# Kernel tuning notes

Measured on AMD Instinct MI355X. Metric: run time of the kernel, lower is better.

Reference implementation:

```python
import jax, jax.numpy as jnp
import numpy as np

B, S, D = 8, 2048, 512
MINF = 20000.0  # matches tf code's -20000.0 mask constant


def setup_inputs() -> dict:
    key = jax.random.key(0)
    k1, k2, k3 = jax.random.split(key, 3)
    x1 = jax.random.normal(k1, (B, S, D), dtype=jnp.float32)
    x2 = jax.random.normal(k2, (B, S, D), dtype=jnp.float32)
    # glorot_normal init for the learned (S, S) positional kernel
    std = np.sqrt(2.0 / (S + S)).astype(np.float32)
    kernel = jax.random.normal(k3, (S, S), dtype=jnp.float32) * std
    return {"x1": x1, "x2": x2, "kernel": kernel}


def reference(x1, x2, kernel):
    S_ = kernel.shape[0]
    # tf.matmul(kernel, inputs[i]) broadcasts (S,S) @ (B,S,D) -> (B,S,D)
    h1 = jnp.einsum('st,btd->bsd', kernel, x1)
    h2 = jnp.einsum('st,btd->bsd', kernel, x2)
    # att_scores: (B, S, S)
    scores = jnp.einsum('bsd,btd->bst', h1, h2)
    d_k = jnp.asarray(S_, dtype=scores.dtype) ** 0.5
    # upper_m[i,j] = -20000 for j > i (strictly upper), else 0; added BEFORE scaling
    row = jnp.arange(S_)
    mask = jnp.where(row[None, :] > row[:, None], -MINF, 0.0).astype(scores.dtype)
    attn = jax.nn.softmax((scores + mask) / d_k, axis=-1)
    # note: output attends over h1 (not h2), as in the original code
    return jnp.einsum('bst,btd->bsd', attn, h1)
```

## Files before the change

kernel.cpp:

```cpp
#include <hip/hip_runtime.h>
#include <hip/hip_bf16.h>

#define S_DIM 2048
#define D_DIM 512
#define B_DIM 8
#define SCALE 0.02209708691207961f

typedef __hip_bfloat16 bf16;
typedef short bf16x8 __attribute__((ext_vector_type(8)));
typedef float f32x4 __attribute__((ext_vector_type(4)));

__device__ __forceinline__ unsigned short f2b(float f) {
  __hip_bfloat16 h = __float2bfloat16(f);
  return __builtin_bit_cast(unsigned short, h);
}
__device__ __forceinline__ float b2f(unsigned short s) {
  return __bfloat162float(__builtin_bit_cast(__hip_bfloat16, s));
}

__device__ __forceinline__ void load_lds16(const void* g, void* l) {
  __builtin_amdgcn_global_load_lds((const __attribute__((address_space(1))) void*)g,
                                   (__attribute__((address_space(3))) void*)l, 16, 0, 0);
}

__global__ void prep(const float* __restrict__ x1, const float* __restrict__ x2,
                     const float* __restrict__ km,
                     bf16* __restrict__ xt, bf16* __restrict__ Kbf,
                     float* __restrict__ rowsum) {
  const int z = blockIdx.z;
  const int tid = threadIdx.x;
  if (z == 16) {
    const int bid = blockIdx.y * 8 + blockIdx.x;
    const float4* p = (const float4*)km;
    bf16x8* o = (bf16x8*)Kbf;
#pragma unroll
    for (int it = 0; it < 8; it++) {
      int i = bid * 2048 + it * 256 + tid;
      float4 a = p[2 * i], b = p[2 * i + 1];
      bf16x8 r;
      r[0] = f2b(a.x); r[1] = f2b(a.y); r[2] = f2b(a.z); r[3] = f2b(a.w);
      r[4] = f2b(b.x); r[5] = f2b(b.y); r[6] = f2b(b.z); r[7] = f2b(b.w);
      o[i] = r;
    }
    if (bid < 8) {
      float4 zf = {0.0f, 0.0f, 0.0f, 0.0f};
      float4* rp = (float4*)(rowsum + bid * 2048);
      rp[tid * 2] = zf;
      rp[tid * 2 + 1] = zf;
    }
    return;
  }
  __shared__ unsigned short t[64][66];
  const float* in = (z < 8 ? x1 : x2) + (size_t)(z & 7) * (S_DIM * D_DIM);
  bf16* ob = xt + (size_t)z * (size_t)(D_DIM * S_DIM);
  const int r0 = blockIdx.y * 64;
  const int c0 = blockIdx.x * 64;
  const int lr = tid >> 4, lq = tid & 15;
#pragma unroll
  for (int i = 0; i < 4; i++) {
    int r = i * 16 + lr;
    float4 v = *(const float4*)(in + (size_t)(r0 + r) * D_DIM + c0 + lq * 4);
    t[lq * 4 + 0][r] = f2b(v.x);
    t[lq * 4 + 1][r] = f2b(v.y);
    t[lq * 4 + 2][r] = f2b(v.z);
    t[lq * 4 + 3][r] = f2b(v.w);
  }
  __syncthreads();
#pragma unroll
  for (int j = 0; j < 4; j++) {
    int d = j * 16 + lr;
    const unsigned short* p = &t[d][lq * 4];
    uint2 u;
    u.x = (unsigned)p[0] | ((unsigned)p[1] << 16);
    u.y = (unsigned)p[2] | ((unsigned)p[3] << 16);
    *(uint2*)(ob + (size_t)(c0 + d) * S_DIM + r0 + lq * 4) = u;
  }
}

__global__ __launch_bounds__(512, 1) void gemm_h(
    const bf16* __restrict__ A, const bf16* __restrict__ X, bf16* __restrict__ H) {
  extern __shared__ char smem[];
  const int pid = blockIdx.x;
  const int mt = pid & 7;
  const int r_ = pid >> 3;
  const int ntile = r_ & 1;
  const int item = r_ >> 1;
  const int m0 = mt * 256, n0 = ntile * 256;
  const bf16* Xi = X + (size_t)item * (D_DIM * S_DIM);
  bf16* Hi = H + (size_t)item * (S_DIM * D_DIM);

  const int tid = threadIdx.x;
  const int w = tid >> 6, L = tid & 63;
  const int l15 = L & 15, lhi = L >> 4;
  const int wr = w >> 2, wn = w & 3;

  const int srow = tid >> 3;
  const int sslot = ((tid & 7) ^ (srow & 7)) * 8;
  const bf16* pA[4];
  const bf16* pB[4];
#pragma unroll
  for (int ld = 0; ld < 4; ld++) {
    pA[ld] = A + (size_t)(m0 + ld * 64 + srow) * 2048 + sslot;
    pB[ld] = Xi + (size_t)(n0 + ld * 64 + srow) * 2048 + sslot;
  }

  auto stage = [&](int t) {
    char* dA = smem + (t & 1) * 32768 + w * 1024;
    char* dB = smem + 65536 + (t & 1) * 32768 + w * 1024;
    const int ko = t * 64;
#pragma unroll
    for (int ld = 0; ld < 4; ld++) {
      load_lds16(pA[ld] + ko, dA + ld * 8192);
      load_lds16(pB[ld] + ko, dB + ld * 8192);
    }
  };

  const int xsw = l15 & 7;
  int offA0[8], offB0[4];
#pragma unroll
  for (int m = 0; m < 8; m++)
    offA0[m] = (wr * 128 + m * 16 + l15) * 128 + ((lhi ^ xsw) << 4);
#pragma unroll
  for (int n = 0; n < 4; n++)
    offB0[n] = (wn * 64 + n * 16 + l15) * 128 + ((lhi ^ xsw) << 4);

  f32x4 acc[8][4];
#pragma unroll
  for (int m = 0; m < 8; m++)
#pragma unroll
    for (int n = 0; n < 4; n++) acc[m][n] = (f32x4){0, 0, 0, 0};

  stage(0);
  asm volatile("s_waitcnt vmcnt(0)" ::: "memory");
  __builtin_amdgcn_s_barrier();
  asm volatile("" ::: "memory");

#pragma unroll 1
  for (int t = 0; t < 32; ++t) {
    if (t + 1 < 32) stage(t + 1);
    const char* bA = smem + (t & 1) * 32768;
    const char* bB = smem + 65536 + (t & 1) * 32768;
#pragma unroll
    for (int kk = 0; kk < 2; kk++) {
      bf16x8 af[8], bfv[4];
#pragma unroll
      for (int m = 0; m < 8; m++) af[m] = *(const bf16x8*)(bA + (offA0[m] ^ (kk << 6)));
#pragma unroll
      for (int n = 0; n < 4; n++) bfv[n] = *(const bf16x8*)(bB + (offB0[n] ^ (kk << 6)));
      __builtin_amdgcn_s_setprio(1);
#pragma unroll
      for (int m = 0; m < 8; m++)
#pragma unroll
        for (int n = 0; n < 4; n++)
          acc[m][n] = __builtin_amdgcn_mfma_f32_16x16x32_bf16(bfv[n], af[m], acc[m][n], 0, 0, 0);
      __builtin_amdgcn_s_setprio(0);
    }
    asm volatile("s_waitcnt vmcnt(0)" ::: "memory");
    __builtin_amdgcn_s_barrier();
    asm volatile("" ::: "memory");
  }

#pragma unroll
  for (int m = 0; m < 8; m++) {
    int grow = m0 + wr * 128 + m * 16 + l15;
#pragma unroll
    for (int n = 0; n < 4; n++) {
      int gcol = n0 + wn * 64 + n * 16 + lhi * 4;
      uint2 u;
      u.x = ((unsigned)f2b(acc[m][n][1]) << 16) | f2b(acc[m][n][0]);
      u.y = ((unsigned)f2b(acc[m][n][3]) << 16) | f2b(acc[m][n][2]);
      *(uint2*)(Hi + (size_t)grow * D_DIM + gcol) = u;
    }
  }
}

__global__ __launch_bounds__(512, 2) void gemm_score(
    const bf16* __restrict__ H1, const bf16* __restrict__ H2,
    bf16* __restrict__ E, float* __restrict__ rowsum, bf16* __restrict__ H1T) {
  extern __shared__ char smem[];
  const int pid = blockIdx.x;
  const int tid = threadIdx.x;

  if (pid >= 288) {
    const int tb = pid - 288;
    const int half = tid >> 8;
    const int t5 = tid & 255;
    unsigned short (*tl)[66] = (unsigned short (*)[66])(smem + half * 8448);
    const int lr = t5 >> 4, lq = t5 & 15;
#pragma unroll 1
    for (int i = 0; i < 4; i++) {
      const int tile = tb * 8 + half * 4 + i;
      const int z = tile >> 8;
      const int rem = tile & 255;
      const int r0 = (rem >> 3) * 64;
      const int c0 = (rem & 7) * 64;
      const bf16* ib = H1 + (size_t)z * (S_DIM * D_DIM);
      bf16* ob = H1T + (size_t)z * (S_DIM * D_DIM);
#pragma unroll
      for (int j = 0; j < 4; j++) {
        int r = j * 16 + lr;
        uint2 v = *(const uint2*)(ib + (size_t)(r0 + r) * D_DIM + c0 + lq * 4);
        tl[lq * 4 + 0][r] = (unsigned short)(v.x & 0xffff);
        tl[lq * 4 + 1][r] = (unsigned short)(v.x >> 16);
        tl[lq * 4 + 2][r] = (unsigned short)(v.y & 0xffff);
        tl[lq * 4 + 3][r] = (unsigned short)(v.y >> 16);
      }
      __syncthreads();
#pragma unroll
      for (int j = 0; j < 4; j++) {
        int d = j * 16 + lr;
        const unsigned short* p = &tl[d][lq * 4];
        uint2 u;
        u.x = (unsigned)p[0] | ((unsigned)p[1] << 16);
        u.y = (unsigned)p[2] | ((unsigned)p[3] << 16);
        *(uint2*)(ob + (size_t)(c0 + d) * S_DIM + r0 + lq * 4) = u;
      }
      __syncthreads();
    }
    return;
  }

  const int b = pid & 7;
  const int tri = pid >> 3;
  int mt = (int)((sqrtf(8.0f * (float)tri + 1.0f) - 1.0f) * 0.5f);
  while ((mt + 1) * (mt + 2) / 2 <= tri) mt++;
  while (mt * (mt + 1) / 2 > tri) mt--;
  const int nt = tri - mt * (mt + 1) / 2;
  const int m0 = mt * 256, n0 = nt * 256;
  const bool diag = (mt == nt);
  const bf16* Ab = H1 + (size_t)b * S_DIM * D_DIM;
  const bf16* Bb = H2 + (size_t)b * S_DIM * D_DIM;
  bf16* Eb = E + (size_t)b * S_DIM * S_DIM;
  float* rs = rowsum + b * S_DIM;

  const int w = tid >> 6, L = tid & 63;
  const int l15 = L & 15, lhi = L >> 4;
  const int wr = w >> 2, wn = w & 3;

  const int srow = tid >> 2;
  const int sslot = ((tid & 3) ^ ((tid >> 3) & 3)) * 8;
  const bf16* pA[2];
  const bf16* pB[2];
#pragma unroll
  for (int ld = 0; ld < 2; ld++) {
    pA[ld] = Ab + (size_t)(m0 + ld * 128 + srow) * D_DIM + sslot;
    pB[ld] = Bb + (size_t)(n0 + ld * 128 + srow) * D_DIM + sslot;
  }

  auto stage = [&](int t) {
    char* dA = smem + (t & 1) * 16384;
    char* dB = smem + 32768 + (t & 1) * 16384;
#pragma unroll
    for (int ld = 0; ld < 2; ld++)
      load_lds16(pA[ld] + t * 32, dA + ld * 8192 + w * 1024);
#pragma unroll
    for (int ld = 0; ld < 2; ld++)
      load_lds16(pB[ld] + t * 32, dB + ld * 8192 + w * 1024);
  };

  const int xo = (lhi ^ ((l15 >> 1) & 3)) << 4;
  int offA[8], offB[4];
#pragma unroll
  for (int m = 0; m < 8; m++) offA[m] = (wr * 128 + m * 16 + l15) * 64 + xo;
#pragma unroll
  for (int n = 0; n < 4; n++) offB[n] = (wn * 64 + n * 16 + l15) * 64 + xo;

  f32x4 acc[8][4];
#pragma unroll
  for (int m = 0; m < 8; m++)
#pragma unroll
    for (int n = 0; n < 4; n++) acc[m][n] = (f32x4){0, 0, 0, 0};

  stage(0);
#pragma unroll 2
  for (int t = 0; t < 16; ++t) {
    __syncthreads();
    if (t + 1 < 16) stage(t + 1);
    const char* bA = smem + (t & 1) * 16384;
    const char* bB = smem + 32768 + (t & 1) * 16384;
    bf16x8 af[8], bfv[4];
#pragma unroll
    for (int m = 0; m < 8; m++) af[m] = *(const bf16x8*)(bA + offA[m]);
#pragma unroll
    for (int n = 0; n < 4; n++) bfv[n] = *(const bf16x8*)(bB + offB[n]);
    __builtin_amdgcn_s_setprio(1);
#pragma unroll
    for (int m = 0; m < 8; m++)
#pragma unroll
      for (int n = 0; n < 4; n++)
        acc[m][n] = __builtin_amdgcn_mfma_f32_16x16x32_bf16(bfv[n], af[m], acc[m][n], 0, 0, 0);
    __builtin_amdgcn_s_setprio(0);
  }

#pragma unroll
  for (int m = 0; m < 8; m++) {
    int sg = m0 + wr * 128 + m * 16 + l15;
    float rp = 0.0f;
#pragma unroll
    for (int n = 0; n < 4; n++) {
      int tg0 = n0 + wn * 64 + n * 16 + lhi * 4;
      unsigned short e[4];
#pragma unroll
      for (int r = 0; r < 4; r++) {
        float v = (!diag || (tg0 + r) <= sg) ? __expf(acc[m][n][r] * SCALE) : 0.0f;
        e[r] = f2b(v);
        rp += b2f(e[r]);
      }
      uint2 u;
      u.x = ((unsigned)e[1] << 16) | e[0];
      u.y = ((unsigned)e[3] << 16) | e[2];
      *(uint2*)(Eb + (size_t)sg * S_DIM + tg0) = u;
    }
    rp += __shfl_xor(rp, 16);
    rp += __shfl_xor(rp, 32);
    if (lhi == 0) atomicAdd(rs + sg, rp);
  }
}

__global__ __launch_bounds__(256, 2) void gemm_pv(
    const bf16* __restrict__ E, const bf16* __restrict__ H1T,
    const float* __restrict__ rowsum, float* __restrict__ out) {
  extern __shared__ char smem[];
  const int pid = blockIdx.x;
  const int b = pid & 7;
  const int r_ = pid >> 3;
  const int nt = r_ & 3;
  const int mb = r_ >> 2;
  const int mt = (mb < 8) ? 2 * mb : 31 - 2 * mb;
  const int m0 = mt * 128, n0 = nt * 128;
  const int NT = (mt + 1) * 4;
  const bf16* Ab = E + (size_t)b * S_DIM * S_DIM + (size_t)m0 * S_DIM;
  const bf16* Bb = H1T + (size_t)b * D_DIM * S_DIM + (size_t)n0 * S_DIM;
  const float* rs = rowsum + b * S_DIM;
  float* Cb = out + (size_t)b * S_DIM * D_DIM;

  const int tid = threadIdx.x;
  const int w = tid >> 6, L = tid & 63;
  const int l15 = L & 15, lhi = L >> 4;
  const int wr = w >> 1, wc = w & 1;

  const int srow = tid >> 2;
  const int sslot = ((tid & 3) ^ ((tid >> 3) & 3)) * 8;
  const bf16* pA[2];
  const bf16* pB[2];
#pragma unroll
  for (int ld = 0; ld < 2; ld++) {
    pA[ld] = Ab + (size_t)(ld * 64 + srow) * S_DIM + sslot;
    pB[ld] = Bb + (size_t)(ld * 64 + srow) * S_DIM + sslot;
  }

  char* A0 = smem;          char* A1 = smem + 8192;   char* A2 = smem + 16384;
  char* B0 = smem + 24576;  char* B1 = smem + 32768;  char* B2 = smem + 40960;

  auto stage = [&](int t2, char* dA, char* dB) {
#pragma unroll
    for (int ld = 0; ld < 2; ld++)
      load_lds16(pA[ld] + t2 * 32, dA + ld * 4096 + w * 1024);
#pragma unroll
    for (int ld = 0; ld < 2; ld++)
      load_lds16(pB[ld] + t2 * 32, dB + ld * 4096 + w * 1024);
  };

  const int xo = (lhi ^ ((l15 >> 1) & 3)) << 4;
  int offA[4], offB[4];
#pragma unroll
  for (int m = 0; m < 4; m++) offA[m] = (wr * 64 + m * 16 + l15) * 64 + xo;
#pragma unroll
  for (int n = 0; n < 4; n++) offB[n] = (wc * 64 + n * 16 + l15) * 64 + xo;

  f32x4 acc[4][4];
#pragma unroll
  for (int m = 0; m < 4; m++)
#pragma unroll
    for (int n = 0; n < 4; n++) acc[m][n] = (f32x4){0, 0, 0, 0};

  stage(0, A0, B0);
  stage(1, A1, B1);

#pragma unroll 1
  for (int t = 0; t < NT; ++t) {
    if (t < NT - 1) asm volatile("s_waitcnt vmcnt(4)" ::: "memory");
    else            asm volatile("s_waitcnt vmcnt(0)" ::: "memory");
    __builtin_amdgcn_s_barrier();
    asm volatile("" ::: "memory");
    if (t + 2 < NT) stage(t + 2, A2, B2);

    bf16x8 af[4], bfv[4];
#pragma unroll
    for (int m = 0; m < 4; m++) af[m] = *(const bf16x8*)(A0 + offA[m]);
#pragma unroll
    for (int n = 0; n < 4; n++) bfv[n] = *(const bf16x8*)(B0 + offB[n]);
    __builtin_amdgcn_s_setprio(1);
#pragma unroll
    for (int m = 0; m < 4; m++)
#pragma unroll
      for (int n = 0; n < 4; n++)
        acc[m][n] = __builtin_amdgcn_mfma_f32_16x16x32_bf16(bfv[n], af[m], acc[m][n], 0, 0, 0);
    __builtin_amdgcn_s_setprio(0);

    char* tA = A0; A0 = A1; A1 = A2; A2 = tA;
    char* tB = B0; B0 = B1; B1 = B2; B2 = tB;
  }

#pragma unroll
  for (int m = 0; m < 4; m++) {
    int sg = m0 + wr * 64 + m * 16 + l15;
    float inv = 1.0f / rs[sg];
#pragma unroll
    for (int n = 0; n < 4; n++) {
      int gcol = n0 + wc * 64 + n * 16 + lhi * 4;
      float4 o;
      o.x = acc[m][n][0] * inv;
      o.y = acc[m][n][1] * inv;
      o.z = acc[m][n][2] * inv;
      o.w = acc[m][n][3] * inv;
      *(float4*)(Cb + (size_t)sg * D_DIM + gcol) = o;
    }
  }
}

extern "C" void kernel_launch(void* const* d_in, const int* in_sizes, int n_in,
                              void* d_out, int out_size, void* d_ws, size_t ws_size,
                              hipStream_t stream) {
  const float* x1 = (const float*)d_in[0];
  const float* x2 = (const float*)d_in[1];
  const float* km = (const float*)d_in[2];
  float* out = (float*)d_out;
  char* ws = (char*)d_ws;
  bf16* E    = (bf16*)(ws);
  bf16* Kbf  = (bf16*)(ws);
  bf16* x1t  = (bf16*)(ws + (8ull << 20));
  bf16* h1n  = (bf16*)(ws + (64ull << 20));
  bf16* h2n  = (bf16*)(ws + (80ull << 20));
  bf16* h1t  = (bf16*)(ws + (96ull << 20));
  float* rowsum = (float*)(ws + (112ull << 20));

  prep<<<dim3(8, 32, 17), 256, 0, stream>>>(x1, x2, km, x1t, Kbf, rowsum);
  gemm_h<<<256, 512, 131072, stream>>>(Kbf, x1t, h1n);
  gemm_score<<<544, 512, 65536, stream>>>(h1n, h2n, E, rowsum, h1t);
  gemm_pv<<<512, 256, 49152, stream>>>(E, h1t, rowsum, out);
}
```

Measured before the change: 163.3 us.

## Use BK=64 double-buffered pipeline in gemm_pv with wider LDS swizzle

The P·V GEMM now stages K-tiles of 64 instead of 32, halving the number of loop iterations and barriers. The triple-buffered BK=32 prefetch is replaced by double buffering, with loads issued before compute and a full vmcnt(0) wait plus barrier at the end of each iteration. The LDS swizzle widens to an 8-slot XOR pattern for 128-byte rows. Shared memory grows from 48 KB to 64 KB per block, and prefetch depth drops to one tile, which may expose more load latency.

```diff
diff --git a/kernel.cpp b/kernel.cpp
--- a/kernel.cpp
+++ b/kernel.cpp
@@ -328,7 +328,7 @@
   const int mb = r_ >> 2;
   const int mt = (mb < 8) ? 2 * mb : 31 - 2 * mb;
   const int m0 = mt * 128, n0 = nt * 128;
-  const int NT = (mt + 1) * 4;
+  const int NT = (mt + 1) * 2;
   const bf16* Ab = E + (size_t)b * S_DIM * S_DIM + (size_t)m0 * S_DIM;
   const bf16* Bb = H1T + (size_t)b * D_DIM * S_DIM + (size_t)n0 * S_DIM;
   const float* rs = rowsum + b * S_DIM;
@@ -339,34 +339,35 @@
   const int l15 = L & 15, lhi = L >> 4;
   const int wr = w >> 1, wc = w & 1;
 
-  const int srow = tid >> 2;
-  const int sslot = ((tid & 3) ^ ((tid >> 3) & 3)) * 8;
-  const bf16* pA[2];
-  const bf16* pB[2];
-#pragma unroll
-  for (int ld = 0; ld < 2; ld++) {
-    pA[ld] = Ab + (size_t)(ld * 64 + srow) * S_DIM + sslot;
-    pB[ld] = Bb + (size_t)(ld * 64 + srow) * S_DIM + sslot;
-  }
-
-  char* A0 = smem;          char* A1 = smem + 8192;   char* A2 = smem + 16384;
-  char* B0 = smem + 24576;  char* B1 = smem + 32768;  char* B2 = smem + 40960;
-
-  auto stage = [&](int t2, char* dA, char* dB) {
-#pragma unroll
-    for (int ld = 0; ld < 2; ld++)
-      load_lds16(pA[ld] + t2 * 32, dA + ld * 4096 + w * 1024);
-#pragma unroll
-    for (int ld = 0; ld < 2; ld++)
-      load_lds16(pB[ld] + t2 * 32, dB + ld * 4096 + w * 1024);
+  const int srow = tid >> 3;
+  const int sslot = ((tid & 7) ^ (srow & 7)) * 8;
+  const bf16* pA[4];
+  const bf16* pB[4];
+#pragma unroll
+  for (int ld = 0; ld < 4; ld++) {
+    pA[ld] = Ab + (size_t)(ld * 32 + srow) * S_DIM + sslot;
+    pB[ld] = Bb + (size_t)(ld * 32 + srow) * S_DIM + sslot;
+  }
+
+  auto stage = [&](int t) {
+    char* dA = smem + (t & 1) * 16384 + w * 1024;
+    char* dB = smem + 32768 + (t & 1) * 16384 + w * 1024;
+    const int ko = t * 64;
+#pragma unroll
+    for (int ld = 0; ld < 4; ld++) {
+      load_lds16(pA[ld] + ko, dA + ld * 4096);
+      load_lds16(pB[ld] + ko, dB + ld * 4096);
+    }
   };
 
-  const int xo = (lhi ^ ((l15 >> 1) & 3)) << 4;
-  int offA[4], offB[4];
-#pragma unroll
-  for (int m = 0; m < 4; m++) offA[m] = (wr * 64 + m * 16 + l15) * 64 + xo;
-#pragma unroll
-  for (int n = 0; n < 4; n++) offB[n] = (wc * 64 + n * 16 + l15) * 64 + xo;
+  const int xsw = l15 & 7;
+  int offA0[4], offB0[4];
+#pragma unroll
+  for (int m = 0; m < 4; m++)
+    offA0[m] = (wr * 64 + m * 16 + l15) * 128 + ((lhi ^ xsw) << 4);
+#pragma unroll
+  for (int n = 0; n < 4; n++)
+    offB0[n] = (wc * 64 + n * 16 + l15) * 128 + ((lhi ^ xsw) << 4);
 
   f32x4 acc[4][4];
 #pragma unroll
@@ -374,32 +375,34 @@
 #pragma unroll
     for (int n = 0; n < 4; n++) acc[m][n] = (f32x4){0, 0, 0, 0};
 
-  stage(0, A0, B0);
-  stage(1, A1, B1);
+  stage(0);
+  asm volatile("s_waitcnt vmcnt(0)" ::: "memory");
+  __builtin_amdgcn_s_barrier();
+  asm volatile("" ::: "memory");
 
 #pragma unroll 1
   for (int t = 0; t < NT; ++t) {
-    if (t < NT - 1) asm volatile("s_waitcnt vmcnt(4)" ::: "memory");
-    else            asm volatile("s_waitcnt vmcnt(0)" ::: "memory");
+    if (t + 1 < NT) stage(t + 1);
+    const char* bA = smem + (t & 1) * 16384;
+    const char* bB = smem + 32768 + (t & 1) * 16384;
+#pragma unroll
+    for (int kk = 0; kk < 2; kk++) {
+      bf16x8 af[4], bfv[4];
+#pragma unroll
+      for (int m = 0; m < 4; m++) af[m] = *(const bf16x8*)(bA + (offA0[m] ^ (kk << 6)));
+#pragma unroll
+      for (int n = 0; n < 4; n++) bfv[n] = *(const bf16x8*)(bB + (offB0[n] ^ (kk << 6)));
+      __builtin_amdgcn_s_setprio(1);
+#pragma unroll
+      for (int m = 0; m < 4; m++)
+#pragma unroll
+        for (int n = 0; n < 4; n++)
+          acc[m][n] = __builtin_amdgcn_mfma_f32_16x16x32_bf16(bfv[n], af[m], acc[m][n], 0, 0, 0);
+      __builtin_amdgcn_s_setprio(0);
+    }
+    asm volatile("s_waitcnt vmcnt(0)" ::: "memory");
     __builtin_amdgcn_s_barrier();
     asm volatile("" ::: "memory");
-    if (t + 2 < NT) stage(t + 2, A2, B2);
-
-    bf16x8 af[4], bfv[4];
-#pragma unroll
-    for (int m = 0; m < 4; m++) af[m] = *(const bf16x8*)(A0 + offA[m]);
-#pragma unroll
-    for (int n = 0; n < 4; n++) bfv[n] = *(const bf16x8*)(B0 + offB[n]);
-    __builtin_amdgcn_s_setprio(1);
-#pragma unroll
-    for (int m = 0; m < 4; m++)
-#pragma unroll
-      for (int n = 0; n < 4; n++)
-        acc[m][n] = __builtin_amdgcn_mfma_f32_16x16x32_bf16(bfv[n], af[m], acc[m][n], 0, 0, 0);
-    __builtin_amdgcn_s_setprio(0);
-
-    char* tA = A0; A0 = A1; A1 = A2; A2 = tA;
-    char* tB = B0; B0 = B1; B1 = B2; B2 = tB;
   }
 
 #pragma unroll
@@ -438,5 +441,5 @@
   prep<<<dim3(8, 32, 17), 256, 0, stream>>>(x1, x2, km, x1t, Kbf, rowsum);
   gemm_h<<<256, 512, 131072, stream>>>(Kbf, x1t, h1n);
   gemm_score<<<544, 512, 65536, stream>>>(h1n, h2n, E, rowsum, h1t);
-  gemm_pv<<<512, 256, 49152, stream>>>(E, h1t, rowsum, out);
-}
+  gemm_pv<<<512, 256, 65536, stream>>>(E, h1t, rowsum, out);
+}
```

Measured after the change: 161.0 us. No clear change (-1.4%).
